# Performance work log

Hardware: AMD Instinct MI355X
Metric: run time of the kernel (lower is better)

The kernel has to match this reference:

```python
import jax, jax.numpy as jnp
import numpy as np

N_HEADS, HEAD_OUT, IN_DIM = 4, 32, 128
HID = N_HEADS * HEAD_OUT  # 128, concat=True
N_NODES, N_EDGES, N_GRAPHS = 50000, 800000, 512
NEG_SLOPE = 0.2


def setup_inputs() -> dict:
    key = jax.random.key(0)
    ks = jax.random.split(key, 8)
    x = jax.random.normal(ks[0], (N_NODES, IN_DIM), jnp.float32)
    edge_index = jax.random.randint(ks[1], (2, N_EDGES), 0, N_NODES, dtype=jnp.int32)
    batch_index = jnp.sort(jax.random.randint(ks[2], (N_NODES,), 0, N_GRAPHS, dtype=jnp.int32))
    s_in = 1.0 / np.sqrt(IN_DIM)
    s_h = 1.0 / np.sqrt(HID)
    W_l = jax.random.normal(ks[3], (IN_DIM, HID), jnp.float32) * s_in   # GATv2 lin_l (source)
    W_r = jax.random.normal(ks[4], (IN_DIM, HID), jnp.float32) * s_in   # GATv2 lin_r (target)
    att = jax.random.normal(ks[5], (N_HEADS, HEAD_OUT), jnp.float32) * (1.0 / np.sqrt(HEAD_OUT))
    bias = jnp.zeros((HID,), jnp.float32)                                # GATv2 output bias
    W_rel = jax.random.normal(ks[6], (HID, 1), jnp.float32) * s_h        # SAGPool GraphConv lin_rel
    b_rel = jnp.zeros((1,), jnp.float32)
    W_root = jax.random.normal(ks[7], (HID, 1), jnp.float32) * s_h       # SAGPool GraphConv lin_root (no bias)
    return dict(x=x, edge_index=edge_index, batch_index=batch_index,
                W_l=W_l, W_r=W_r, att=att, bias=bias,
                W_rel=W_rel, b_rel=b_rel, W_root=W_root)


def _segment_softmax(logits, seg, num_segments):
    m = jax.ops.segment_max(logits, seg, num_segments=num_segments)
    m = jnp.where(jnp.isfinite(m), m, 0.0)
    e = jnp.exp(logits - m[seg])
    d = jax.ops.segment_sum(e, seg, num_segments=num_segments)
    return e / jnp.maximum(d[seg], 1e-16)


def _forward(x, edge_index, batch_index, W_l, W_r, att, bias, W_rel, b_rel, W_root):
    N = x.shape[0]
    src0, dst0 = edge_index[0], edge_index[1]
    # --- GATv2Conv (add_self_loops=True default) ---
    loop = jnp.arange(N, dtype=src0.dtype)
    src = jnp.concatenate([src0, loop])
    dst = jnp.concatenate([dst0, loop])
    xl = (x @ W_l).reshape(N, N_HEADS, HEAD_OUT)  # source transform
    xr = (x @ W_r).reshape(N, N_HEADS, HEAD_OUT)  # target transform
    e = jax.nn.leaky_relu(xl[src] + xr[dst], NEG_SLOPE)          # [E+N, H, C]
    logits = jnp.einsum('ehc,hc->eh', e, att)                     # [E+N, H]
    alpha = _segment_softmax(logits, dst, N)                      # neighborhood softmax per dst
    out = jax.ops.segment_sum(xl[src] * alpha[:, :, None], dst, num_segments=N)
    out = out.reshape(N, HID) + bias                              # concat heads + bias
    # --- SAGPooling(min_score=-1): GraphConv score -> per-graph softmax; all nodes kept ---
    agg = jax.ops.segment_sum(out[src0], dst0, num_segments=N)    # add-aggregate neighbors
    score = (agg @ W_rel + b_rel + out @ W_root).squeeze(-1)      # [N]
    s = _segment_softmax(score, batch_index, N_GRAPHS)            # softmax over each graph
    att_x = out * s[:, None]
    # --- global_add_pool ---
    g = jax.ops.segment_sum(att_x, batch_index, num_segments=N_GRAPHS)  # [B, HID]
    return out, g


def reference(x, edge_index, batch_index, W_l, W_r, att, bias, W_rel, b_rel, W_root):
    return _forward(x, edge_index, batch_index, W_l, W_r, att, bias, W_rel, b_rel, W_root)
```

## Files before the change

kernel.cpp:

```cpp
#include <hip/hip_runtime.h>
#include <cfloat>

#define N_NODES 50000
#define E0      800000
#define EP      850000
#define NGRAPH  512
#define HID     128
#define NB_SCAN 49
#define NEG_SLOPE 0.2f
#define GTILE   32

__global__ __launch_bounds__(256) void k_hist(const int* __restrict__ dst0, int* __restrict__ cnt){
  int e = blockIdx.x*256 + threadIdx.x;
  if (e < E0) atomicAdd(&cnt[dst0[e]], 1);
}

__global__ __launch_bounds__(256) void k_scan1(const int* __restrict__ cnt, int* __restrict__ bsum){
  __shared__ int red[256];
  int tid = threadIdx.x;
  int base = blockIdx.x*1024 + tid*4;
  int s = 0;
  #pragma unroll
  for (int i=0;i<4;++i){ int idx = base+i; if (idx < N_NODES) s += cnt[idx] + 1; }
  red[tid] = s; __syncthreads();
  for (int off=128; off>0; off>>=1){ if (tid<off) red[tid]+=red[tid+off]; __syncthreads(); }
  if (tid==0) bsum[blockIdx.x] = red[0];
}

__global__ void k_scan2(const int* __restrict__ bsum, int* __restrict__ boff, int* __restrict__ row_start){
  if (threadIdx.x == 0){
    int run = 0;
    for (int b=0;b<NB_SCAN;++b){ boff[b] = run; run += bsum[b]; }
    row_start[N_NODES] = run;
  }
}

__global__ __launch_bounds__(256) void k_scan3(const int* __restrict__ cnt, const int* __restrict__ boff,
    int* __restrict__ row_start, int* __restrict__ fill){
  __shared__ int sbuf[256];
  int tid = threadIdx.x;
  int base = blockIdx.x*1024 + tid*4;
  int v[4]; int ts = 0;
  #pragma unroll
  for (int i=0;i<4;++i){ int idx=base+i; v[i] = (idx<N_NODES)? cnt[idx]+1 : 0; ts += v[i]; }
  sbuf[tid] = ts; __syncthreads();
  for (int off=1; off<256; off<<=1){
    int add = (tid>=off)? sbuf[tid-off] : 0;
    __syncthreads();
    sbuf[tid] += add;
    __syncthreads();
  }
  int run = boff[blockIdx.x] + sbuf[tid] - ts;
  #pragma unroll
  for (int i=0;i<4;++i){
    int idx = base+i;
    if (idx < N_NODES){ row_start[idx]=run; fill[idx]=run; run += v[i]; }
  }
}

__global__ __launch_bounds__(256) void k_scatter(const int* __restrict__ src0, const int* __restrict__ dst0,
    int* __restrict__ fill, int* __restrict__ col_src){
  int i = blockIdx.x*256 + threadIdx.x;
  if (i >= EP) return;
  int s, d;
  if (i < E0){ s = src0[i]; d = dst0[i]; }
  else       { s = i - E0;  d = s; }
  int slot = atomicAdd(&fill[d], 1);
  col_src[slot] = s;
}

__global__ __launch_bounds__(128) void k_gemm(const float* __restrict__ x,
    const float* __restrict__ Wl, const float* __restrict__ Wr,
    float* __restrict__ xl, float* __restrict__ xr){
  __shared__ float xs[GTILE][128];
  int tid = threadIdx.x;
  int n0 = blockIdx.x * GTILE;
  #pragma unroll
  for (int it=0; it<8; ++it){
    int f = it*512 + tid*4;
    int r = f >> 7, c = f & 127;
    float4 v = make_float4(0.f,0.f,0.f,0.f);
    if (n0 + r < N_NODES) v = *(const float4*)&x[(size_t)(n0+r)*128 + c];
    *(float4*)&xs[r][c] = v;
  }
  __syncthreads();
  int cgrp = tid & 31, ngrp = tid >> 5;
  int c4 = cgrp*4;
  float accl[8][4], accr[8][4];
  #pragma unroll
  for (int i=0;i<8;++i)
    #pragma unroll
    for (int j=0;j<4;++j){ accl[i][j]=0.f; accr[i][j]=0.f; }

  for (int k=0; k<128; k+=4){
    float4 a4[8];
    #pragma unroll
    for (int i=0;i<8;++i) a4[i] = *(const float4*)&xs[ngrp*8+i][k];
    float4 wl4[4], wr4[4];
    #pragma unroll
    for (int kk=0;kk<4;++kk){
      wl4[kk] = *(const float4*)&Wl[(size_t)(k+kk)*128 + c4];
      wr4[kk] = *(const float4*)&Wr[(size_t)(k+kk)*128 + c4];
    }
    #pragma unroll
    for (int i=0;i<8;++i){
      const float* av = (const float*)&a4[i];
      #pragma unroll
      for (int kk=0;kk<4;++kk){
        float a = av[kk];
        const float* wl = (const float*)&wl4[kk];
        const float* wr = (const float*)&wr4[kk];
        #pragma unroll
        for (int j=0;j<4;++j){
          accl[i][j] = fmaf(a, wl[j], accl[i][j]);
          accr[i][j] = fmaf(a, wr[j], accr[i][j]);
        }
      }
    }
  }
  #pragma unroll
  for (int i=0;i<8;++i){
    int node = n0 + ngrp*8 + i;
    if (node < N_NODES){
      float4 vl = make_float4(accl[i][0], accl[i][1], accl[i][2], accl[i][3]);
      float4 vr = make_float4(accr[i][0], accr[i][1], accr[i][2], accr[i][3]);
      *(float4*)&xl[(size_t)node*128 + c4] = vl;
      *(float4*)&xr[(size_t)node*128 + c4] = vr;
    }
  }
}

__device__ __forceinline__ float lrdot(float2 v, float2 xr2, float2 at2){
  float ex = v.x + xr2.x, ey = v.y + xr2.y;
  ex = ex > 0.f ? ex : NEG_SLOPE*ex;
  ey = ey > 0.f ? ey : NEG_SLOPE*ey;
  return ex*at2.x + ey*at2.y;
}

__global__ __launch_bounds__(256) void k_attn(
    const float* __restrict__ xl, const float* __restrict__ xr,
    const int* __restrict__ row_start, const int* __restrict__ col_src,
    const float* __restrict__ attv, const float* __restrict__ bias,
    const float* __restrict__ Wrel, const float* __restrict__ Wroot,
    const float* __restrict__ brel,
    float* __restrict__ out, float* __restrict__ pbuf, float* __restrict__ score){
  int wid = blockIdx.x*4 + (threadIdx.x >> 6);
  if (wid >= N_NODES) return;
  int lane = threadIdx.x & 63;
  int c2 = lane*2;
  float2 xr2 = *(const float2*)&xr[(size_t)wid*128 + c2];
  float2 at2 = *(const float2*)&attv[c2];
  int row = row_start[wid];
  int deg = row_start[wid+1] - row;
  float d = 0.f, ax = 0.f, ay = 0.f;
  int i = 0;
  for (; i+4 <= deg; i += 4){
    int s0 = col_src[row+i+0];
    int s1 = col_src[row+i+1];
    int s2 = col_src[row+i+2];
    int s3 = col_src[row+i+3];
    float2 v0 = *(const float2*)&xl[(size_t)s0*128 + c2];
    float2 v1 = *(const float2*)&xl[(size_t)s1*128 + c2];
    float2 v2 = *(const float2*)&xl[(size_t)s2*128 + c2];
    float2 v3 = *(const float2*)&xl[(size_t)s3*128 + c2];
    float t0 = lrdot(v0, xr2, at2);
    float t1 = lrdot(v1, xr2, at2);
    float t2 = lrdot(v2, xr2, at2);
    float t3 = lrdot(v3, xr2, at2);
    t0 += __shfl_xor(t0,1); t1 += __shfl_xor(t1,1); t2 += __shfl_xor(t2,1); t3 += __shfl_xor(t3,1);
    t0 += __shfl_xor(t0,2); t1 += __shfl_xor(t1,2); t2 += __shfl_xor(t2,2); t3 += __shfl_xor(t3,2);
    t0 += __shfl_xor(t0,4); t1 += __shfl_xor(t1,4); t2 += __shfl_xor(t2,4); t3 += __shfl_xor(t3,4);
    t0 += __shfl_xor(t0,8); t1 += __shfl_xor(t1,8); t2 += __shfl_xor(t2,8); t3 += __shfl_xor(t3,8);
    float w0 = __expf(t0), w1 = __expf(t1), w2 = __expf(t2), w3 = __expf(t3);
    d += (w0 + w1) + (w2 + w3);
    ax = fmaf(w3, v3.x, fmaf(w2, v2.x, fmaf(w1, v1.x, fmaf(w0, v0.x, ax))));
    ay = fmaf(w3, v3.y, fmaf(w2, v2.y, fmaf(w1, v1.y, fmaf(w0, v0.y, ay))));
  }
  for (; i < deg; ++i){
    int s = col_src[row+i];
    float2 v = *(const float2*)&xl[(size_t)s*128 + c2];
    float t = lrdot(v, xr2, at2);
    t += __shfl_xor(t,1); t += __shfl_xor(t,2); t += __shfl_xor(t,4); t += __shfl_xor(t,8);
    float w = __expf(t);
    d += w;
    ax = fmaf(w, v.x, ax);
    ay = fmaf(w, v.y, ay);
  }
  float inv = 1.f/d;
  float ox = fmaf(ax, inv, bias[c2]);
  float oy = fmaf(ay, inv, bias[c2+1]);
  *(float2*)&out[(size_t)wid*128 + c2] = make_float2(ox, oy);
  float pv = ox*Wrel[c2]  + oy*Wrel[c2+1];
  float rv = ox*Wroot[c2] + oy*Wroot[c2+1];
  #pragma unroll
  for (int off=1; off<64; off<<=1){
    pv += __shfl_xor(pv, off);
    rv += __shfl_xor(rv, off);
  }
  if (lane == 0){
    pbuf[wid]  = pv;
    score[wid] = brel[0] + rv;
  }
}

__global__ __launch_bounds__(256) void k_score(
    const int* __restrict__ row_start, const int* __restrict__ col_src,
    const float* __restrict__ pbuf, float* __restrict__ score){
  int n = blockIdx.x*256 + threadIdx.x;
  if (n >= N_NODES) return;
  int row = row_start[n], deg = row_start[n+1]-row;
  float sc = score[n] - pbuf[n];
  for (int i=0;i<deg;++i) sc += pbuf[col_src[row+i]];
  score[n] = sc;
}

__device__ __forceinline__ int lbound(const int* __restrict__ a, int n, int v){
  int lo=0, hi=n;
  while (lo < hi){ int mid=(lo+hi)>>1; if (a[mid] < v) lo = mid+1; else hi = mid; }
  return lo;
}

__global__ __launch_bounds__(128) void k_pool(
    const int* __restrict__ batch, const float* __restrict__ score,
    const float* __restrict__ out, float* __restrict__ g){
  int b = blockIdx.x;
  int tid = threadIdx.x;
  int start = lbound(batch, N_NODES, b);
  int end   = lbound(batch, N_NODES, b+1);
  __shared__ float red[128];
  __shared__ float sl[128];
  float lm = -FLT_MAX;
  for (int i=start+tid; i<end; i+=128) lm = fmaxf(lm, score[i]);
  red[tid]=lm; __syncthreads();
  for (int off=64; off>0; off>>=1){ if (tid<off) red[tid]=fmaxf(red[tid],red[tid+off]); __syncthreads(); }
  float m = red[0]; __syncthreads();
  float ls = 0.f;
  for (int i=start+tid; i<end; i+=128) ls += __expf(score[i]-m);
  red[tid]=ls; __syncthreads();
  for (int off=64; off>0; off>>=1){ if (tid<off) red[tid]+=red[tid+off]; __syncthreads(); }
  float inv = 1.f / fmaxf(red[0], 1e-16f);
  __syncthreads();
  float acc = 0.f;
  for (int base=start; base<end; base+=128){
    int idx = base+tid;
    sl[tid] = (idx<end) ? __expf(score[idx]-m)*inv : 0.f;
    __syncthreads();
    int lim = min(128, end-base);
    for (int jj=0; jj<lim; ++jj) acc = fmaf(out[(size_t)(base+jj)*128 + tid], sl[jj], acc);
    __syncthreads();
  }
  g[b*128 + tid] = acc;
}

extern "C" void kernel_launch(void* const* d_in, const int* in_sizes, int n_in,
                              void* d_out, int out_size, void* d_ws, size_t ws_size,
                              hipStream_t stream){
  const float* x    = (const float*)d_in[0];
  const int*   ei   = (const int*)d_in[1];
  const int*   batch= (const int*)d_in[2];
  const float* Wl   = (const float*)d_in[3];
  const float* Wr   = (const float*)d_in[4];
  const float* attv = (const float*)d_in[5];
  const float* bias = (const float*)d_in[6];
  const float* Wrel = (const float*)d_in[7];
  const float* brel = (const float*)d_in[8];
  const float* Wroot= (const float*)d_in[9];
  const int* src0 = ei;
  const int* dst0 = ei + E0;

  float* out = (float*)d_out;
  float* g   = out + (size_t)N_NODES*HID;

  float* xl = (float*)d_ws;
  float* xr = xl + (size_t)N_NODES*HID;
  int* cnt       = (int*)(xr + (size_t)N_NODES*HID);
  int* row_start = cnt + N_NODES;
  int* fill      = row_start + N_NODES + 1;
  int* bsum      = fill + N_NODES;
  int* boff      = bsum + NB_SCAN;
  int* col_src   = boff + NB_SCAN;
  float* pbuf    = (float*)(col_src + EP);
  float* score   = pbuf + N_NODES;

  hipMemsetAsync(cnt, 0, N_NODES*sizeof(int), stream);
  k_gemm   <<<dim3((N_NODES+GTILE-1)/GTILE), 128, 0, stream>>>(x, Wl, Wr, xl, xr);
  k_hist   <<<dim3((E0+255)/256),    256, 0, stream>>>(dst0, cnt);
  k_scan1  <<<dim3(NB_SCAN),         256, 0, stream>>>(cnt, bsum);
  k_scan2  <<<dim3(1),                64, 0, stream>>>(bsum, boff, row_start);
  k_scan3  <<<dim3(NB_SCAN),         256, 0, stream>>>(cnt, boff, row_start, fill);
  k_scatter<<<dim3((EP+255)/256),    256, 0, stream>>>(src0, dst0, fill, col_src);
  k_attn   <<<dim3(N_NODES/4),       256, 0, stream>>>(xl, xr, row_start, col_src,
                                                       attv, bias, Wrel, Wroot, brel,
                                                       out, pbuf, score);
  k_score  <<<dim3((N_NODES+255)/256),256, 0, stream>>>(row_start, col_src, pbuf, score);
  k_pool   <<<dim3(NGRAPH),          128, 0, stream>>>(batch, score, out, g);
}
```

Measured before the change: 337.2 us.

## Merge scan kernels, double-buffer GEMM weights, use DPP reductions, edge-parallel score

Replaces the three-kernel prefix scan with a single 1024-thread block scan, which removes two launches but serialises the scan onto one CU. The GEMM now double-buffers the weight loads in registers and requests 2 blocks per CU through launch bounds. The attention logit reduction uses DPP lane ops instead of shuffles. The score aggregation switches from a per-node CSR gather loop to per-edge float atomics, which makes the float summation order nondeterministic.

```diff
diff --git a/kernel.cpp b/kernel.cpp
--- a/kernel.cpp
+++ b/kernel.cpp
@@ -6,56 +6,35 @@
 #define EP      850000
 #define NGRAPH  512
 #define HID     128
-#define NB_SCAN 49
 #define NEG_SLOPE 0.2f
 #define GTILE   32
+#define SCHUNK  49
 
 __global__ __launch_bounds__(256) void k_hist(const int* __restrict__ dst0, int* __restrict__ cnt){
   int e = blockIdx.x*256 + threadIdx.x;
   if (e < E0) atomicAdd(&cnt[dst0[e]], 1);
 }
 
-__global__ __launch_bounds__(256) void k_scan1(const int* __restrict__ cnt, int* __restrict__ bsum){
-  __shared__ int red[256];
+__global__ __launch_bounds__(1024) void k_scan_all(const int* __restrict__ cnt,
+    int* __restrict__ row_start, int* __restrict__ fill){
+  __shared__ int sbuf[1024];
   int tid = threadIdx.x;
-  int base = blockIdx.x*1024 + tid*4;
+  int base = tid*SCHUNK;
   int s = 0;
-  #pragma unroll
-  for (int i=0;i<4;++i){ int idx = base+i; if (idx < N_NODES) s += cnt[idx] + 1; }
-  red[tid] = s; __syncthreads();
-  for (int off=128; off>0; off>>=1){ if (tid<off) red[tid]+=red[tid+off]; __syncthreads(); }
-  if (tid==0) bsum[blockIdx.x] = red[0];
-}
-
-__global__ void k_scan2(const int* __restrict__ bsum, int* __restrict__ boff, int* __restrict__ row_start){
-  if (threadIdx.x == 0){
-    int run = 0;
-    for (int b=0;b<NB_SCAN;++b){ boff[b] = run; run += bsum[b]; }
-    row_start[N_NODES] = run;
-  }
-}
-
-__global__ __launch_bounds__(256) void k_scan3(const int* __restrict__ cnt, const int* __restrict__ boff,
-    int* __restrict__ row_start, int* __restrict__ fill){
-  __shared__ int sbuf[256];
-  int tid = threadIdx.x;
-  int base = blockIdx.x*1024 + tid*4;
-  int v[4]; int ts = 0;
-  #pragma unroll
-  for (int i=0;i<4;++i){ int idx=base+i; v[i] = (idx<N_NODES)? cnt[idx]+1 : 0; ts += v[i]; }
-  sbuf[tid] = ts; __syncthreads();
-  for (int off=1; off<256; off<<=1){
+  for (int i=0;i<SCHUNK;++i){ int idx=base+i; if (idx<N_NODES) s += cnt[idx]+1; }
+  sbuf[tid] = s; __syncthreads();
+  for (int off=1; off<1024; off<<=1){
     int add = (tid>=off)? sbuf[tid-off] : 0;
     __syncthreads();
     sbuf[tid] += add;
     __syncthreads();
   }
-  int run = boff[blockIdx.x] + sbuf[tid] - ts;
-  #pragma unroll
-  for (int i=0;i<4;++i){
-    int idx = base+i;
-    if (idx < N_NODES){ row_start[idx]=run; fill[idx]=run; run += v[i]; }
-  }
+  int run = sbuf[tid] - s;
+  for (int i=0;i<SCHUNK;++i){
+    int idx=base+i;
+    if (idx<N_NODES){ row_start[idx]=run; fill[idx]=run; run += cnt[idx]+1; }
+  }
+  if (tid==1023) row_start[N_NODES] = sbuf[1023];
 }
 
 __global__ __launch_bounds__(256) void k_scatter(const int* __restrict__ src0, const int* __restrict__ dst0,
@@ -69,7 +48,29 @@
   col_src[slot] = s;
 }
 
-__global__ __launch_bounds__(128) void k_gemm(const float* __restrict__ x,
+#define GEMM_CHUNK(KB, WLB, WRB)                                            \
+  {                                                                         \
+    float4 a4[8];                                                           \
+    _Pragma("unroll")                                                       \
+    for (int i2=0;i2<8;++i2) a4[i2] = *(const float4*)&xs[ngrp*8+i2][KB];   \
+    _Pragma("unroll")                                                       \
+    for (int i2=0;i2<8;++i2){                                               \
+      const float* av = (const float*)&a4[i2];                              \
+      _Pragma("unroll")                                                     \
+      for (int kk2=0;kk2<4;++kk2){                                          \
+        float a = av[kk2];                                                  \
+        const float* pl = (const float*)&WLB[kk2];                          \
+        const float* pr = (const float*)&WRB[kk2];                          \
+        _Pragma("unroll")                                                   \
+        for (int j2=0;j2<4;++j2){                                           \
+          accl[i2][j2] = fmaf(a, pl[j2], accl[i2][j2]);                     \
+          accr[i2][j2] = fmaf(a, pr[j2], accr[i2][j2]);                     \
+        }                                                                   \
+      }                                                                     \
+    }                                                                       \
+  }
+
+__global__ __launch_bounds__(128, 2) void k_gemm(const float* __restrict__ x,
     const float* __restrict__ Wl, const float* __restrict__ Wr,
     float* __restrict__ xl, float* __restrict__ xr){
   __shared__ float xs[GTILE][128];
@@ -86,37 +87,35 @@
   __syncthreads();
   int cgrp = tid & 31, ngrp = tid >> 5;
   int c4 = cgrp*4;
+  const float* Wlp = Wl + c4;
+  const float* Wrp = Wr + c4;
   float accl[8][4], accr[8][4];
   #pragma unroll
   for (int i=0;i<8;++i)
     #pragma unroll
     for (int j=0;j<4;++j){ accl[i][j]=0.f; accr[i][j]=0.f; }
 
-  for (int k=0; k<128; k+=4){
-    float4 a4[8];
-    #pragma unroll
-    for (int i=0;i<8;++i) a4[i] = *(const float4*)&xs[ngrp*8+i][k];
-    float4 wl4[4], wr4[4];
+  float4 wlA[4], wrA[4], wlB[4], wrB[4];
+  #pragma unroll
+  for (int kk=0;kk<4;++kk){
+    wlA[kk] = *(const float4*)&Wlp[(size_t)kk*128];
+    wrA[kk] = *(const float4*)&Wrp[(size_t)kk*128];
+  }
+  for (int k=0; k<128; k+=8){
     #pragma unroll
     for (int kk=0;kk<4;++kk){
-      wl4[kk] = *(const float4*)&Wl[(size_t)(k+kk)*128 + c4];
-      wr4[kk] = *(const float4*)&Wr[(size_t)(k+kk)*128 + c4];
+      wlB[kk] = *(const float4*)&Wlp[(size_t)(k+4+kk)*128];
+      wrB[kk] = *(const float4*)&Wrp[(size_t)(k+4+kk)*128];
     }
-    #pragma unroll
-    for (int i=0;i<8;++i){
-      const float* av = (const float*)&a4[i];
+    GEMM_CHUNK(k, wlA, wrA)
+    if (k+8 < 128){
       #pragma unroll
       for (int kk=0;kk<4;++kk){
-        float a = av[kk];
-        const float* wl = (const float*)&wl4[kk];
-        const float* wr = (const float*)&wr4[kk];
-        #pragma unroll
-        for (int j=0;j<4;++j){
-          accl[i][j] = fmaf(a, wl[j], accl[i][j]);
-          accr[i][j] = fmaf(a, wr[j], accr[i][j]);
-        }
+        wlA[kk] = *(const float4*)&Wlp[(size_t)(k+8+kk)*128];
+        wrA[kk] = *(const float4*)&Wrp[(size_t)(k+8+kk)*128];
       }
     }
+    GEMM_CHUNK(k+4, wlB, wrB)
   }
   #pragma unroll
   for (int i=0;i<8;++i){
@@ -128,6 +127,16 @@
       *(float4*)&xr[(size_t)node*128 + c4] = vr;
     }
   }
+}
+
+#define DPP_ADD(x, ctrl) ((x) + __int_as_float(__builtin_amdgcn_update_dpp( \
+    0, __float_as_int(x), (ctrl), 0xf, 0xf, true)))
+__device__ __forceinline__ float red16(float t){
+  t = DPP_ADD(t, 0xB1);
+  t = DPP_ADD(t, 0x4E);
+  t = DPP_ADD(t, 0x141);
+  t = DPP_ADD(t, 0x140);
+  return t;
 }
 
 __device__ __forceinline__ float lrdot(float2 v, float2 xr2, float2 at2){
@@ -163,14 +172,10 @@
     float2 v1 = *(const float2*)&xl[(size_t)s1*128 + c2];
     float2 v2 = *(const float2*)&xl[(size_t)s2*128 + c2];
     float2 v3 = *(const float2*)&xl[(size_t)s3*128 + c2];
-    float t0 = lrdot(v0, xr2, at2);
-    float t1 = lrdot(v1, xr2, at2);
-    float t2 = lrdot(v2, xr2, at2);
-    float t3 = lrdot(v3, xr2, at2);
-    t0 += __shfl_xor(t0,1); t1 += __shfl_xor(t1,1); t2 += __shfl_xor(t2,1); t3 += __shfl_xor(t3,1);
-    t0 += __shfl_xor(t0,2); t1 += __shfl_xor(t1,2); t2 += __shfl_xor(t2,2); t3 += __shfl_xor(t3,2);
-    t0 += __shfl_xor(t0,4); t1 += __shfl_xor(t1,4); t2 += __shfl_xor(t2,4); t3 += __shfl_xor(t3,4);
-    t0 += __shfl_xor(t0,8); t1 += __shfl_xor(t1,8); t2 += __shfl_xor(t2,8); t3 += __shfl_xor(t3,8);
+    float t0 = red16(lrdot(v0, xr2, at2));
+    float t1 = red16(lrdot(v1, xr2, at2));
+    float t2 = red16(lrdot(v2, xr2, at2));
+    float t3 = red16(lrdot(v3, xr2, at2));
     float w0 = __expf(t0), w1 = __expf(t1), w2 = __expf(t2), w3 = __expf(t3);
     d += (w0 + w1) + (w2 + w3);
     ax = fmaf(w3, v3.x, fmaf(w2, v2.x, fmaf(w1, v1.x, fmaf(w0, v0.x, ax))));
@@ -179,8 +184,7 @@
   for (; i < deg; ++i){
     int s = col_src[row+i];
     float2 v = *(const float2*)&xl[(size_t)s*128 + c2];
-    float t = lrdot(v, xr2, at2);
-    t += __shfl_xor(t,1); t += __shfl_xor(t,2); t += __shfl_xor(t,4); t += __shfl_xor(t,8);
+    float t = red16(lrdot(v, xr2, at2));
     float w = __expf(t);
     d += w;
     ax = fmaf(w, v.x, ax);
@@ -203,15 +207,11 @@
   }
 }
 
-__global__ __launch_bounds__(256) void k_score(
-    const int* __restrict__ row_start, const int* __restrict__ col_src,
+__global__ __launch_bounds__(256) void k_score_edges(
+    const int* __restrict__ src0, const int* __restrict__ dst0,
     const float* __restrict__ pbuf, float* __restrict__ score){
-  int n = blockIdx.x*256 + threadIdx.x;
-  if (n >= N_NODES) return;
-  int row = row_start[n], deg = row_start[n+1]-row;
-  float sc = score[n] - pbuf[n];
-  for (int i=0;i<deg;++i) sc += pbuf[col_src[row+i]];
-  score[n] = sc;
+  int e = blockIdx.x*256 + threadIdx.x;
+  if (e < E0) atomicAdd(&score[dst0[e]], pbuf[src0[e]]);
 }
 
 __device__ __forceinline__ int lbound(const int* __restrict__ a, int n, int v){
@@ -276,22 +276,18 @@
   int* cnt       = (int*)(xr + (size_t)N_NODES*HID);
   int* row_start = cnt + N_NODES;
   int* fill      = row_start + N_NODES + 1;
-  int* bsum      = fill + N_NODES;
-  int* boff      = bsum + NB_SCAN;
-  int* col_src   = boff + NB_SCAN;
+  int* col_src   = fill + N_NODES;
   float* pbuf    = (float*)(col_src + EP);
   float* score   = pbuf + N_NODES;
 
   hipMemsetAsync(cnt, 0, N_NODES*sizeof(int), stream);
-  k_gemm   <<<dim3((N_NODES+GTILE-1)/GTILE), 128, 0, stream>>>(x, Wl, Wr, xl, xr);
-  k_hist   <<<dim3((E0+255)/256),    256, 0, stream>>>(dst0, cnt);
-  k_scan1  <<<dim3(NB_SCAN),         256, 0, stream>>>(cnt, bsum);
-  k_scan2  <<<dim3(1),                64, 0, stream>>>(bsum, boff, row_start);
-  k_scan3  <<<dim3(NB_SCAN),         256, 0, stream>>>(cnt, boff, row_start, fill);
-  k_scatter<<<dim3((EP+255)/256),    256, 0, stream>>>(src0, dst0, fill, col_src);
-  k_attn   <<<dim3(N_NODES/4),       256, 0, stream>>>(xl, xr, row_start, col_src,
-                                                       attv, bias, Wrel, Wroot, brel,
-                                                       out, pbuf, score);
-  k_score  <<<dim3((N_NODES+255)/256),256, 0, stream>>>(row_start, col_src, pbuf, score);
-  k_pool   <<<dim3(NGRAPH),          128, 0, stream>>>(batch, score, out, g);
-}
+  k_gemm       <<<dim3((N_NODES+GTILE-1)/GTILE), 128, 0, stream>>>(x, Wl, Wr, xl, xr);
+  k_hist       <<<dim3((E0+255)/256),   256, 0, stream>>>(dst0, cnt);
+  k_scan_all   <<<dim3(1),             1024, 0, stream>>>(cnt, row_start, fill);
+  k_scatter    <<<dim3((EP+255)/256),   256, 0, stream>>>(src0, dst0, fill, col_src);
+  k_attn       <<<dim3(N_NODES/4),      256, 0, stream>>>(xl, xr, row_start, col_src,
+                                                          attv, bias, Wrel, Wroot, brel,
+                                                          out, pbuf, score);
+  k_score_edges<<<dim3((E0+255)/256),   256, 0, stream>>>(src0, dst0, pbuf, score);
+  k_pool       <<<dim3(NGRAPH),         128, 0, stream>>>(batch, score, out, g);
+}
```

After: 474.9 us. +40.9%, slower.
